# Performance work log

Measured on AMD Instinct MI355X. Metric: run time of the kernel, lower is better.

## Reference

```python
import jax, jax.numpy as jnp
import numpy as np

DN = ('NCDHW', 'OIDHW', 'NCDHW')

def conv3d(x, w, b, stride=1, padding=1, lhs_dilation=1):
    pad = [(padding, padding)] * 3 if isinstance(padding, int) else padding
    y = jax.lax.conv_general_dilated(
        x, w, window_strides=(stride,) * 3, padding=pad,
        lhs_dilation=(lhs_dilation,) * 3, dimension_numbers=DN)
    return y + b[None, :, None, None, None]

def bool_to_multichannel(x):
    # (B,1,D,H,W) bool -> (B,8,D/4,H/4,W/4) float; each 4x4x4 patch bit-packed to 8 bytes
    B = x.shape[0]; D = x.shape[2]; d = D // 4
    p = x.reshape(B, d, 4, d, 4, d, 4)
    p = p.transpose(0, 1, 3, 5, 2, 4, 6).reshape(B, d, d, d, 8, 8)
    pw2 = (2.0 ** jnp.arange(8)).astype(jnp.float32)
    mc = jnp.sum(p.astype(jnp.float32) * pw2, axis=-1)  # (B,d,d,d,8)
    return mc.transpose(0, 4, 1, 2, 3) / 255.0

def setup_inputs():
    key = jax.random.key(0)
    ks = jax.random.split(key, 26)
    B, RES = 4, 256
    CH, E, ZC, K = 32, 16, 128, 8192
    L = 16  # latent resolution (mc res 64 / 2^(len(ch_mult)-1))
    # block-sparse boolean voxels so a good fraction of latent patches is all-zero
    coarse = jax.random.uniform(ks[0], (B, 1, 16, 16, 16)) < 0.6
    coarse = jnp.repeat(jnp.repeat(jnp.repeat(coarse, 16, 2), 16, 3), 16, 4)
    dense = jax.random.uniform(ks[1], (B, 1, RES, RES, RES)) < 0.3
    x = coarse & dense
    p = lambda k, shape, s=0.05: (jax.random.normal(k, shape) * s).astype(jnp.float32)
    return {
        'x': x,
        'enc_in_w': p(ks[2], (CH, 8, 3, 3, 3)), 'enc_in_b': p(ks[3], (CH,)),
        'enc_d1_w': p(ks[4], (2 * CH, CH, 3, 3, 3)), 'enc_d1_b': p(ks[5], (2 * CH,)),
        'enc_d2_w': p(ks[6], (4 * CH, 2 * CH, 3, 3, 3)), 'enc_d2_b': p(ks[7], (4 * CH,)),
        'enc_out_w': p(ks[8], (ZC, 4 * CH, 3, 3, 3)), 'enc_out_b': p(ks[9], (ZC,)),
        'quant_w': p(ks[10], (E, ZC, 1, 1, 1)), 'quant_b': p(ks[11], (E,)),
        'codebook': p(ks[12], (K, E), 0.5),
        'replacement_token': p(ks[13], (1, E), 0.02),
        'pos_embedding': p(ks[14], (1, E, L, L, L), 1.0),
        'post_quant_w': p(ks[15], (ZC, E, 1, 1, 1)), 'post_quant_b': p(ks[16], (ZC,)),
        'dec_in_w': p(ks[17], (ZC, ZC, 3, 3, 3)), 'dec_in_b': p(ks[18], (ZC,)),
        'dec_u1_w': p(ks[19], (2 * CH, ZC, 3, 3, 3)), 'dec_u1_b': p(ks[20], (2 * CH,)),
        'dec_u2_w': p(ks[21], (CH, 2 * CH, 3, 3, 3)), 'dec_u2_b': p(ks[22], (CH,)),
        'dec_out_w': p(ks[23], (8, CH, 3, 3, 3)), 'dec_out_b': p(ks[24], (8,)),
    }

def reference(x, enc_in_w, enc_in_b, enc_d1_w, enc_d1_b, enc_d2_w, enc_d2_b,
              enc_out_w, enc_out_b, quant_w, quant_b, codebook, replacement_token,
              pos_embedding, post_quant_w, post_quant_b, dec_in_w, dec_in_b,
              dec_u1_w, dec_u1_b, dec_u2_w, dec_u2_b, dec_out_w, dec_out_b):
    silu = jax.nn.silu
    mc = bool_to_multichannel(x)                      # (B,8,64,64,64)
    B, _, Dm, _, _ = mc.shape
    L = Dm // 4                                       # latent res = 16

    # zero-patch mask, patch_size=4 (== max_pool3d(nonzero_any) < 0.5)
    nz = jnp.any(mc != 0, axis=1)                     # (B,64,64,64)
    pooled = nz.reshape(B, L, 4, L, 4, L, 4).any(axis=(2, 4, 6))
    zero_mask = ~pooled.reshape(B, L * L * L)         # (B,N) True = all-zero patch

    # encoder (downsample x4) + quant_conv (1x1x1)
    h = silu(conv3d(mc, enc_in_w, enc_in_b))
    h = silu(conv3d(h, enc_d1_w, enc_d1_b, stride=2))
    h = silu(conv3d(h, enc_d2_w, enc_d2_b, stride=2))
    h = conv3d(h, enc_out_w, enc_out_b)
    h = conv3d(h, quant_w, quant_b, padding=0)        # (B,E,L,L,L)
    E = h.shape[1]
    seq = h.reshape(B, E, -1).transpose(0, 2, 1)      # (B,N,E)

    dist = jnp.sum(codebook * codebook, axis=-1) - 2.0 * jnp.einsum('bne,ke->bnk', seq, codebook)
    idx = jnp.argmin(dist, axis=-1)                   # (B,N)
    q_nz = codebook[idx]                              # (B,N,E)
    nonzero = ~zero_mask
    # commit over nonzero tokens * non_mask_frac == masked mean over all tokens
    mse_tok = jnp.mean(jnp.square(jax.lax.stop_gradient(q_nz) - seq), axis=-1)
    commit_loss = 0.25 * jnp.mean(jnp.where(nonzero, mse_tok, 0.0))

    # replacement token is index 0 of the full codebook; real codes shift by +1
    full_idx = jnp.where(zero_mask, 0, idx + 1)       # (B,N)
    full_cb = jnp.concatenate([replacement_token, codebook], axis=0)
    quant = full_cb[full_idx].transpose(0, 2, 1).reshape(B, E, L, L, L)

    # decoder (upsample x4 via fractionally-strided convs)
    q = quant + pos_embedding
    q = conv3d(q, post_quant_w, post_quant_b, padding=0)
    d = silu(conv3d(q, dec_in_w, dec_in_b))
    d = silu(conv3d(d, dec_u1_w, dec_u1_b, padding=[(2, 1)] * 3, lhs_dilation=2))
    d = silu(conv3d(d, dec_u2_w, dec_u2_b, padding=[(2, 1)] * 3, lhs_dilation=2))
    recon = conv3d(d, dec_out_w, dec_out_b)           # (B,8,64,64,64)
    return recon, mc, commit_loss, full_idx
```

## Files before the change

kernel.cpp:

```cpp
#include <hip/hip_runtime.h>
#include <hip/hip_bf16.h>
#include <math.h>

#define BB 4
#define NTOK 4096
#define KCB 8192
#define ED 16

__device__ __forceinline__ float silu_f(float x){ return x / (1.0f + expf(-x)); }
__device__ __forceinline__ double silu_d(double x){ return x / (1.0 + exp(-x)); }

template<typename T> struct V4T { typedef T type __attribute__((ext_vector_type(4))); };
typedef float f2v __attribute__((ext_vector_type(2)));

__global__ void r9_probe_zero(int* flags){ if (threadIdx.x < 2) flags[threadIdx.x] = 0; }

__global__ void r17_probe(const unsigned char* __restrict__ x, int* __restrict__ flags){
  __shared__ int so, sa;
  if (threadIdx.x == 0){ so = 0; sa = 0; }
  __syncthreads();
  const uint4* p = (const uint4*)x + (size_t)(blockIdx.x*256 + threadIdx.x)*4;
  unsigned uo = 0, ua = 0;
  #pragma unroll
  for (int r=0;r<4;++r){
    uint4 v = p[r];
    unsigned uw = v.x | v.y | v.z | v.w;
    uo |= (uw & 0xFFFFFF00u);
    ua |= (uw & 0x000000FFu);
  }
  if (uo) so = 1;
  if (ua) sa = 1;
  __syncthreads();
  if (threadIdx.x == 0){
    if (so) atomicOr(flags + 0, 1);
    if (sa) atomicOr(flags + 1, 1);
  }
}

__global__ void r9_pack_mc(const unsigned char* __restrict__ x, float* __restrict__ mc,
                           const int* __restrict__ flags){
  int t = blockIdx.x*256 + threadIdx.x;
  int k = t & 63, j = (t>>6)&63, i = (t>>12)&63, b = t>>18;
  int is_i32 = (flags[1] != 0) && (flags[0] == 0);
  unsigned ch[8];
  #pragma unroll
  for (int q=0;q<8;++q) ch[q]=0u;
  if (is_i32){
    const int* xb = (const int*)x + ((size_t)b << 24);
    #pragma unroll
    for (int a=0;a<4;++a){
      #pragma unroll
      for (int b2=0;b2<4;++b2){
        const int4 v = *(const int4*)(xb + (((size_t)(4*i+a))<<16) + ((size_t)(4*j+b2)<<8) + (size_t)(4*k));
        int vv[4] = {v.x, v.y, v.z, v.w};
        #pragma unroll
        for (int c2=0;c2<4;++c2){
          int lin = a*16 + b2*4 + c2;
          unsigned bit = vv[c2] ? 1u : 0u;
          ch[lin>>3] += bit << (lin&7);
        }
      }
    }
  } else {
    const unsigned char* xb = x + ((size_t)b << 24);
    #pragma unroll
    for (int a=0;a<4;++a){
      #pragma unroll
      for (int b2=0;b2<4;++b2){
        const unsigned char* row = xb + (((size_t)(4*i+a))<<16) + ((size_t)(4*j+b2)<<8) + (size_t)(4*k);
        unsigned v = *(const unsigned*)row;
        #pragma unroll
        for (int c2=0;c2<4;++c2){
          int lin = a*16 + b2*4 + c2;
          unsigned bit = ((v >> (8*c2)) & 0xffu) ? 1u : 0u;
          ch[lin>>3] += bit << (lin&7);
        }
      }
    }
  }
  size_t sp = ((size_t)i<<12) + (j<<6) + k;
  #pragma unroll
  for (int q=0;q<8;++q)
    mc[(((size_t)(b*8+q))<<18) + sp] = (float)ch[q] / 255.0f;
}

__global__ void r9_token_nz(const float* __restrict__ mc, unsigned char* __restrict__ tnz){
  int t = blockIdx.x*64 + threadIdx.x;
  int tk = t&15, tj=(t>>4)&15, ti=(t>>8)&15, b=t>>12;
  bool any = false;
  for (int q=0;q<8 && !any;++q){
    const float* mq = mc + (((size_t)(b*8+q))<<18);
    for (int a=0;a<4;++a)
      for (int c=0;c<4;++c){
        const float4 v = *(const float4*)(mq + ((size_t)(4*ti+a)<<12) + ((size_t)(4*tj+c)<<6) + (size_t)(4*tk));
        if (v.x!=0.f || v.y!=0.f || v.z!=0.f || v.w!=0.f){ any = true; }
      }
  }
  tnz[t] = any ? 1 : 0;
}

template<int XT, int STRIDE, typename TIN, typename ACC>
__device__ __forceinline__ void load_span(const TIN* __restrict__ inr, bool xlo, bool xhi,
                                          ACC (&xv)[STRIDE*(XT-1)+3]){
  static_assert(XT==4, "XT must be 4");
  typedef typename V4T<TIN>::type tin4;
  if (STRIDE==1){
    tin4 m = *(const tin4*)(inr + 1);
    xv[1]=(ACC)m.x; xv[2]=(ACC)m.y; xv[3]=(ACC)m.z; xv[4]=(ACC)m.w;
    xv[0] = xlo ? (ACC)inr[0] : (ACC)0;
    xv[5] = xhi ? (ACC)inr[5] : (ACC)0;
  } else {
    tin4 a = *(const tin4*)(inr + 1);
    tin4 b = *(const tin4*)(inr + 5);
    xv[1]=(ACC)a.x; xv[2]=(ACC)a.y; xv[3]=(ACC)a.z; xv[4]=(ACC)a.w;
    xv[5]=(ACC)b.x; xv[6]=(ACC)b.y; xv[7]=(ACC)b.z; xv[8]=(ACC)b.w;
    xv[0] = xlo ? (ACC)inr[0] : (ACC)0;
  }
}

template<int CIN, int OCB, int XT, int STRIDE, bool DOSILU, typename TIN, typename TOUT, typename ACC>
__global__ void r16_conv3x3(const TIN* __restrict__ in, const float* __restrict__ w,
                            const float* __restrict__ bias, TOUT* __restrict__ out,
                            int Din, int Dout){
  constexpr int SPAN = STRIDE*(XT-1)+3;
  const int oc0 = blockIdx.y * OCB;
  const int n3 = Dout*Dout*Dout;
  const int nxt = Dout / XT;
  const int t = blockIdx.x*256 + threadIdx.x;
  const int xo0 = (t % nxt)*XT;
  const int yo = (t/nxt)%Dout, zo = t/(nxt*Dout);
  const int zi0 = zo*STRIDE-1, yi0 = yo*STRIDE-1, xi0 = xo0*STRIDE-1;
  const bool xlo = (xi0 >= 0);
  const bool xhi = (xi0 + (SPAN-1) < Din);

  ACC acc[OCB][XT];
  #pragma unroll
  for (int q=0;q<OCB;++q){
    ACC bv = (ACC)bias[oc0+q];
    #pragma unroll
    for (int s=0;s<XT;++s) acc[q][s] = bv;
  }

  #pragma unroll 1
  for (int i=0;i<CIN;++i){
    const TIN* inc = in + (size_t)i*Din*Din*Din;
    const float* wci = w + ((size_t)oc0*CIN + i)*27;
    #pragma unroll
    for (int kd=0;kd<3;++kd){
      int z = zi0+kd; if ((unsigned)z >= (unsigned)Din) continue;
      #pragma unroll
      for (int kh=0;kh<3;++kh){
        int y = yi0+kh; if ((unsigned)y >= (unsigned)Din) continue;
        const TIN* inr = inc + ((size_t)z*Din + y)*Din + xi0;
        ACC xv[SPAN];
        load_span<XT,STRIDE,TIN,ACC>(inr, xlo, xhi, xv);
        #pragma unroll
        for (int q=0;q<OCB;++q){
          const float* wr = wci + (size_t)q*CIN*27 + kd*9 + kh*3;
          #pragma unroll
          for (int kw=0;kw<3;++kw){
            ACC wv = (ACC)wr[kw];
            #pragma unroll
            for (int s=0;s<XT;++s)
              acc[q][s] = fma(wv, xv[s*STRIDE+kw], acc[q][s]);
          }
        }
      }
    }
  }
  if (DOSILU){
    #pragma unroll
    for (int q=0;q<OCB;++q)
      #pragma unroll
      for (int s=0;s<XT;++s){
        if (sizeof(ACC)==8) acc[q][s] = (ACC)silu_d((double)acc[q][s]);
        else                acc[q][s] = (ACC)silu_f((float)acc[q][s]);
      }
  }
  size_t vox = ((size_t)zo*Dout + yo)*Dout + xo0;
  #pragma unroll
  for (int q=0;q<OCB;++q)
    #pragma unroll
    for (int s=0;s<XT;++s)
      out[(size_t)(oc0+q)*n3 + vox + s] = (TOUT)acc[q][s];
}

template<int CIN, int OCB, int XT, int NS, int STRIDE, typename TIN, typename ACC>
__global__ void r16_conv_part(const TIN* __restrict__ in, const float* __restrict__ w,
                              const float* __restrict__ bias, ACC* __restrict__ part,
                              int Din, int Dout){
  constexpr int SPAN = STRIDE*(XT-1)+3;
  const int oc0 = blockIdx.y * OCB;
  const int OC  = gridDim.y * OCB;
  const int cz  = blockIdx.z;
  const int n3 = Dout*Dout*Dout;
  const int nxt = Dout / XT;
  const int t = blockIdx.x*256 + threadIdx.x;
  const int xo0 = (t % nxt)*XT;
  const int yo = (t/nxt)%Dout, zo = t/(nxt*Dout);
  const int zi0 = zo*STRIDE-1, yi0 = yo*STRIDE-1, xi0 = xo0*STRIDE-1;
  const bool xlo = (xi0 >= 0);
  const bool xhi = (xi0 + (SPAN-1) < Din);

  ACC acc[OCB][XT];
  #pragma unroll
  for (int q=0;q<OCB;++q){
    ACC bv = (cz==0) ? (ACC)bias[oc0+q] : (ACC)0;
    #pragma unroll
    for (int s=0;s<XT;++s) acc[q][s] = bv;
  }

  const int cbeg = cz * (CIN/NS);
  #pragma unroll 1
  for (int i=cbeg; i<cbeg + CIN/NS; ++i){
    const TIN* inc = in + (size_t)i*Din*Din*Din;
    const float* wci = w + ((size_t)oc0*CIN + i)*27;
    #pragma unroll
    for (int kd=0;kd<3;++kd){
      int z = zi0+kd; if ((unsigned)z >= (unsigned)Din) continue;
      #pragma unroll
      for (int kh=0;kh<3;++kh){
        int y = yi0+kh; if ((unsigned)y >= (unsigned)Din) continue;
        const TIN* inr = inc + ((size_t)z*Din + y)*Din + xi0;
        ACC xv[SPAN];
        load_span<XT,STRIDE,TIN,ACC>(inr, xlo, xhi, xv);
        #pragma unroll
        for (int q=0;q<OCB;++q){
          const float* wr = wci + (size_t)q*CIN*27 + kd*9 + kh*3;
          #pragma unroll
          for (int kw=0;kw<3;++kw){
            ACC wv = (ACC)wr[kw];
            #pragma unroll
            for (int s=0;s<XT;++s)
              acc[q][s] = fma(wv, xv[s*STRIDE+kw], acc[q][s]);
          }
        }
      }
    }
  }
  size_t vox = ((size_t)zo*Dout + yo)*Dout + xo0;
  #pragma unroll
  for (int q=0;q<OCB;++q)
    #pragma unroll
    for (int s=0;s<XT;++s)
      part[((size_t)cz*OC + (oc0+q))*n3 + vox + s] = acc[q][s];
}

template<int NS, int VEC, bool DOSILU, typename ACC, typename TOUT>
__global__ void r16_reduce(const ACC* __restrict__ part, TOUT* __restrict__ out, int total){
  int t0 = (blockIdx.x*256 + threadIdx.x)*VEC;
  if (t0 >= total) return;
  ACC a[VEC];
  #pragma unroll
  for (int v=0;v<VEC;++v) a[v] = part[t0+v];
  #pragma unroll
  for (int s=1;s<NS;++s){
    #pragma unroll
    for (int v=0;v<VEC;++v) a[v] += part[(size_t)s*total + t0+v];
  }
  #pragma unroll
  for (int v=0;v<VEC;++v){
    if (DOSILU){
      if (sizeof(ACC)==8) a[v] = (ACC)silu_d((double)a[v]);
      else                a[v] = (ACC)silu_f((float)a[v]);
    }
    out[t0+v] = (TOUT)a[v];
  }
}

__global__ void r9_quantconv_b(const double* __restrict__ h4b, const float* __restrict__ w,
                               const float* __restrict__ bias, double* __restrict__ seqd, int b){
  int t = blockIdx.x*256 + threadIdx.x;
  if (t >= 65536) return;
  int n = t & 4095, e = t >> 12;
  double acc = (double)bias[e];
  const float* we = w + e*128;
  for (int i=0;i<128;++i) acc = fma(h4b[((size_t)i<<12)+n], (double)we[i], acc);
  seqd[((size_t)(b*NTOK+n))*ED + e] = acc;
}

__global__ void r9_postquant_b(const float* __restrict__ qpeb, const float* __restrict__ w,
                               const float* __restrict__ bias, float* __restrict__ pqb){
  int t = blockIdx.x*256 + threadIdx.x;
  if (t >= 524288) return;
  int n = t & 4095, o = t >> 12;
  float acc = bias[o];
  const float* wo = w + o*16;
  #pragma unroll
  for (int e=0;e<16;++e) acc = fmaf(qpeb[((size_t)e<<12)+n], wo[e], acc);
  pqb[t] = acc;
}

__global__ void r9_cnorm(const float* __restrict__ cb, double* __restrict__ cnormd){
  int k = blockIdx.x*256 + threadIdx.x;
  if (k >= KCB) return;
  const float* c = cb + (size_t)k*ED;
  double s = 0.0;
  #pragma unroll
  for (int e=0;e<ED;++e) s = fma((double)c[e], (double)c[e], s);
  cnormd[k] = s;
}

#define VQC 256
#define VQPARTS 16
template<int PARTS>
__global__ void r12_vq_partial(const double* __restrict__ seqd, const float* __restrict__ cb,
                               const double* __restrict__ cnormd,
                               double* __restrict__ pdist, int* __restrict__ pidx){
  __shared__ double scb[VQC*ED];
  __shared__ double snorm[VQC];
  int part = blockIdx.y;
  int tok = blockIdx.x*256 + threadIdx.x;
  double s[16];
  const double* sr = seqd + (size_t)tok*ED;
  #pragma unroll
  for (int e=0;e<16;++e) s[e] = sr[e];
  double best = 1.0e300; int bi = 0;
  const int CP = KCB/PARTS;
  for (int c=0;c<CP/VQC;++c){
    int kbase = part*CP + c*VQC;
    for (int u=threadIdx.x; u<VQC*ED; u+=256) scb[u] = (double)cb[(size_t)kbase*ED + u];
    for (int u=threadIdx.x; u<VQC; u+=256) snorm[u] = cnormd[kbase+u];
    __syncthreads();
    for (int kk=0; kk<VQC; ++kk){
      const double* cr = scb + kk*ED;
      double dot = 0.0;
      #pragma unroll
      for (int e=0;e<16;++e) dot = fma(s[e], cr[e], dot);
      double dist = snorm[kk] - 2.0*dot;
      if (dist < best){ best = dist; bi = kbase+kk; }
    }
    __syncthreads();
  }
  pdist[part*16384 + tok] = best;
  pidx [part*16384 + tok] = bi;
}

template<int PARTS>
__global__ void r12_vq_merge(const double* __restrict__ pdist, const int* __restrict__ pidx,
                             const unsigned char* __restrict__ tnz, int* __restrict__ idxw,
                             float* __restrict__ out_idx, float* __restrict__ loss_slot){
  int tok = blockIdx.x*256 + threadIdx.x;
  if (tok == 0) *loss_slot = 0.f;
  double best = pdist[tok]; int bi = pidx[tok];
  #pragma unroll
  for (int p=1;p<PARTS;++p){
    double d2 = pdist[p*16384+tok];
    if (d2 < best){ best = d2; bi = pidx[p*16384+tok]; }
  }
  idxw[tok] = bi;
  out_idx[tok] = tnz[tok] ? (float)(bi+1) : 0.f;
}

__global__ void r9_commit(const double* __restrict__ seqd, const float* __restrict__ cb,
                          const int* __restrict__ idxw, const unsigned char* __restrict__ tnz,
                          float* __restrict__ loss_slot){
  int tok = blockIdx.x*256 + threadIdx.x;
  float v = 0.f;
  if (tnz[tok]){
    const float* c = cb + (size_t)idxw[tok]*ED;
    const double* s = seqd + (size_t)tok*ED;
    double acc = 0.0;
    #pragma unroll
    for (int e=0;e<ED;++e){ double d = (double)c[e]-s[e]; acc = fma(d,d,acc); }
    v = (float)(acc * (0.25/(16.0*16384.0)));
  }
  #pragma unroll
  for (int off=32; off; off>>=1) v += __shfl_down(v, off);
  if ((threadIdx.x & 63) == 0) atomicAdd(loss_slot, v);
}

__global__ void r9_gather_pos(const float* __restrict__ cb, const float* __restrict__ rep,
                              const int* __restrict__ idxw, const unsigned char* __restrict__ tnz,
                              const float* __restrict__ pos, float* __restrict__ qpe){
  int t = blockIdx.x*256 + threadIdx.x;
  int n = t & 4095, e = (t>>12)&15, b = t>>16;
  int tok = b*NTOK + n;
  float v = tnz[tok] ? cb[(size_t)idxw[tok]*ED + e] : rep[e];
  qpe[t] = v + pos[((size_t)e<<12) + n];
}

template<int CIN, int XT, bool DOSILU>
__global__ void r16_tconv(const float* __restrict__ in, const float* __restrict__ w,
                          const float* __restrict__ bias, float* __restrict__ out,
                          int Din){
  static_assert(XT==2, "XT must be 2");
  const int oc = blockIdx.y;
  const int nxt = Din / XT;
  const int t = blockIdx.x*256 + threadIdx.x;
  const int ux0 = (t % nxt)*XT;
  const int uy = (t/nxt)%Din, uz = t/(nxt*Din);
  const bool vx = ux0 > 0, vy = uy > 0, vz = uz > 0;
  const int DD = Din*Din, n3 = DD*Din;

  float b0 = bias[oc];
  float acc[8][XT];
  #pragma unroll
  for (int q=0;q<8;++q)
    #pragma unroll
    for (int s=0;s<XT;++s) acc[q][s] = b0;

  const float* p = in + ((size_t)uz*Din + uy)*Din + ux0;
  #pragma unroll 1
  for (int i=0;i<CIN;++i){
    float X[2][2][XT+1];
    #pragma unroll
    for (int za=0; za<2; ++za){
      #pragma unroll
      for (int ya=0; ya<2; ++ya){
        bool okzy = (za==1 || vz) && (ya==1 || vy);
        const float* pr = p + (za-1)*DD + (ya-1)*Din;
        if (okzy){
          f2v m = *(const f2v*)(pr);
          X[za][ya][1] = m.x; X[za][ya][2] = m.y;
          X[za][ya][0] = vx ? pr[-1] : 0.f;
        } else {
          X[za][ya][0] = 0.f; X[za][ya][1] = 0.f; X[za][ya][2] = 0.f;
        }
      }
    }
    const float* wi = w + ((size_t)(oc*CIN) + i)*27;
    #pragma unroll
    for (int kd=0;kd<3;++kd){
      #pragma unroll
      for (int kh=0;kh<3;++kh){
        #pragma unroll
        for (int kw=0;kw<3;++kw){
          const int pz = (kd==1) ? 1 : 0, py = (kh==1) ? 1 : 0, px = (kw==1) ? 1 : 0;
          const int za = (kd==0) ? 0 : 1, ya = (kh==0) ? 0 : 1, xa = (kw==0) ? 0 : 1;
          float wv = wi[kd*9+kh*3+kw];
          #pragma unroll
          for (int s=0;s<XT;++s)
            acc[pz*4+py*2+px][s] = fmaf(wv, X[za][ya][s+xa], acc[pz*4+py*2+px][s]);
        }
      }
    }
    p += n3;
  }
  if (DOSILU){
    #pragma unroll
    for (int q=0;q<8;++q)
      #pragma unroll
      for (int s=0;s<XT;++s) acc[q][s] = silu_f(acc[q][s]);
  }
  const int Dout = 2*Din;
  #pragma unroll
  for (int pz=0; pz<2; ++pz){
    #pragma unroll
    for (int py=0; py<2; ++py){
      float* row = out + (((size_t)oc*Dout + 2*uz+pz)*Dout + (2*uy+py))*Dout + 2*ux0;
      #pragma unroll
      for (int s=0;s<XT;++s){
        float2 v2 = make_float2(acc[pz*4+py*2+0][s], acc[pz*4+py*2+1][s]);
        *(float2*)(row + 2*s) = v2;
      }
    }
  }
}

template<int CIN, int XT, int NS>
__global__ void r16_tconv_part(const float* __restrict__ in, const float* __restrict__ w,
                               const float* __restrict__ bias, float* __restrict__ part,
                               int Din){
  static_assert(XT==2, "XT must be 2");
  const int oc = blockIdx.y;
  const int OC = gridDim.y;
  const int cz = blockIdx.z;
  const int nxt = Din / XT;
  const int t = blockIdx.x*256 + threadIdx.x;
  const int ux0 = (t % nxt)*XT;
  const int uy = (t/nxt)%Din, uz = t/(nxt*Din);
  const bool vx = ux0 > 0, vy = uy > 0, vz = uz > 0;
  const int DD = Din*Din, n3 = DD*Din;

  float b0 = (cz==0) ? bias[oc] : 0.f;
  float acc[8][XT];
  #pragma unroll
  for (int q=0;q<8;++q)
    #pragma unroll
    for (int s=0;s<XT;++s) acc[q][s] = b0;

  const int cbeg = cz * (CIN/NS);
  const float* p = in + (size_t)cbeg*n3 + ((size_t)uz*Din + uy)*Din + ux0;
  #pragma unroll 1
  for (int i=cbeg; i<cbeg + CIN/NS; ++i){
    float X[2][2][XT+1];
    #pragma unroll
    for (int za=0; za<2; ++za){
      #pragma unroll
      for (int ya=0; ya<2; ++ya){
        bool okzy = (za==1 || vz) && (ya==1 || vy);
        const float* pr = p + (za-1)*DD + (ya-1)*Din;
        if (okzy){
          f2v m = *(const f2v*)(pr);
          X[za][ya][1] = m.x; X[za][ya][2] = m.y;
          X[za][ya][0] = vx ? pr[-1] : 0.f;
        } else {
          X[za][ya][0] = 0.f; X[za][ya][1] = 0.f; X[za][ya][2] = 0.f;
        }
      }
    }
    const float* wi = w + ((size_t)(oc*CIN) + i)*27;
    #pragma unroll
    for (int kd=0;kd<3;++kd){
      #pragma unroll
      for (int kh=0;kh<3;++kh){
        #pragma unroll
        for (int kw=0;kw<3;++kw){
          const int pz = (kd==1) ? 1 : 0, py = (kh==1) ? 1 : 0, px = (kw==1) ? 1 : 0;
          const int za = (kd==0) ? 0 : 1, ya = (kh==0) ? 0 : 1, xa = (kw==0) ? 0 : 1;
          float wv = wi[kd*9+kh*3+kw];
          #pragma unroll
          for (int s=0;s<XT;++s)
            acc[pz*4+py*2+px][s] = fmaf(wv, X[za][ya][s+xa], acc[pz*4+py*2+px][s]);
        }
      }
    }
    p += n3;
  }
  const int Dout = 2*Din;
  const size_t n3out = (size_t)Dout*Dout*Dout;
  float* pb = part + (size_t)cz*OC*n3out;
  #pragma unroll
  for (int pz=0; pz<2; ++pz){
    #pragma unroll
    for (int py=0; py<2; ++py){
      float* row = pb + (((size_t)oc*Dout + 2*uz+pz)*Dout + (2*uy+py))*Dout + 2*ux0;
      #pragma unroll
      for (int s=0;s<XT;++s){
        float2 v2 = make_float2(acc[pz*4+py*2+0][s], acc[pz*4+py*2+1][s]);
        *(float2*)(row + 2*s) = v2;
      }
    }
  }
}

__global__ void r9_diag_ws(float* out0, float v){
  if (threadIdx.x == 0 && blockIdx.x == 0) out0[0] = v;
}

extern "C" void kernel_launch(void* const* d_in, const int* in_sizes, int n_in,
                              void* d_out, int out_size, void* d_ws, size_t ws_size,
                              hipStream_t stream){
  const unsigned char* x = (const unsigned char*)d_in[0];
  const float* enc_in_w  = (const float*)d_in[1];
  const float* enc_in_b  = (const float*)d_in[2];
  const float* enc_d1_w  = (const float*)d_in[3];
  const float* enc_d1_b  = (const float*)d_in[4];
  const float* enc_d2_w  = (const float*)d_in[5];
  const float* enc_d2_b  = (const float*)d_in[6];
  const float* enc_out_w = (const float*)d_in[7];
  const float* enc_out_b = (const float*)d_in[8];
  const float* quant_w   = (const float*)d_in[9];
  const float* quant_b   = (const float*)d_in[10];
  const float* codebook  = (const float*)d_in[11];
  const float* rep_tok   = (const float*)d_in[12];
  const float* pos_emb   = (const float*)d_in[13];
  const float* pq_w      = (const float*)d_in[14];
  const float* pq_b      = (const float*)d_in[15];
  const float* dec_in_w  = (const float*)d_in[16];
  const float* dec_in_b  = (const float*)d_in[17];
  const float* dec_u1_w  = (const float*)d_in[18];
  const float* dec_u1_b  = (const float*)d_in[19];
  const float* dec_u2_w  = (const float*)d_in[20];
  const float* dec_u2_b  = (const float*)d_in[21];
  const float* dec_out_w = (const float*)d_in[22];
  const float* dec_out_b = (const float*)d_in[23];

  float* out = (float*)d_out;
  const size_t OFF_RECON = 0;
  const size_t OFF_MC    = 8388608;
  const size_t OFF_LOSS  = 16777216;
  const size_t OFF_IDX   = 16777217;

  char* wsb = (char*)d_ws;
  float*  Sbig  = (float*) (wsb + 0);
  float*  Shd   = (float*) (wsb + 33554432);
  double* Sc1   = (double*)(wsb + 41943040);
  double* Sc2   = (double*)(wsb + 46137344);
  float*  Spq   = (float*) (wsb + 50331648);
  float*  SdD   = (float*) (wsb + 52428800);
  double* seqd  = (double*)(wsb + 54525952);
  double* cnormd= (double*)(wsb + 56623104);
  int*    idxw  = (int*)   (wsb + 57475072);
  unsigned char* tnz = (unsigned char*)(wsb + 57540608);
  float*  qpe   = (float*) (wsb + 57556992);
  int*    dflag = (int*)   (wsb + 58605568);
  const size_t WS_NEEDED = 58605632;

  double* scr_d  = (double*)wsb;
  float*  scr_f  = (float*)wsb;
  float*  scr_f2 = (float*)(wsb + 33554432);
  double* pdist  = (double*)wsb;
  int*    pidx   = (int*)(wsb + VQPARTS*16384*8);

  dim3 blk(256);

  if (ws_size < WS_NEEDED){
    r9_diag_ws<<<dim3(1), dim3(64), 0, stream>>>(out + OFF_RECON,
        9.0e6f + (float)(ws_size >> 20));
    return;
  }

  r9_probe_zero<<<dim3(1), dim3(64), 0, stream>>>(dflag);
  r17_probe<<<dim3(256), blk, 0, stream>>>(x, dflag);

  r9_pack_mc<<<dim3(4096), blk, 0, stream>>>(x, out + OFF_MC, dflag);
  r9_token_nz<<<dim3(256), dim3(64), 0, stream>>>(out + OFF_MC, tnz);

  for (int b = 0; b < BB; ++b){
    const float* mcb = out + OFF_MC + (size_t)b*8*262144;
    r16_conv3x3<8,8,4,1,true,float,float,double>  <<<dim3(256,4,1), blk, 0, stream>>>(mcb,  enc_in_w, enc_in_b, Sbig, 64, 64);
    r16_conv3x3<32,4,4,2,true,float,float,double> <<<dim3(32,16,1), blk, 0, stream>>>(Sbig, enc_d1_w, enc_d1_b, Shd,  64, 32);
    r16_conv_part<64,4,4,4,2,float,double><<<dim3(4,32,4), blk, 0, stream>>>(Shd, enc_d2_w, enc_d2_b, scr_d, 32, 16);
    r16_reduce<4,2,true,double,double><<<dim3(1024), blk, 0, stream>>>(scr_d, Sc1, 524288);
    r16_conv_part<128,4,4,8,1,double,double><<<dim3(4,32,8), blk, 0, stream>>>(Sc1, enc_out_w, enc_out_b, scr_d, 16, 16);
    r16_reduce<8,2,false,double,double><<<dim3(1024), blk, 0, stream>>>(scr_d, Sc2, 524288);
    r9_quantconv_b<<<dim3(256), blk, 0, stream>>>(Sc2, quant_w, quant_b, seqd, b);
  }

  r9_cnorm<<<dim3(32), blk, 0, stream>>>(codebook, cnormd);
  r12_vq_partial<VQPARTS><<<dim3(64,VQPARTS), blk, 0, stream>>>(seqd, codebook, cnormd, pdist, pidx);
  r12_vq_merge<VQPARTS><<<dim3(64), blk, 0, stream>>>(pdist, pidx, tnz, idxw, out + OFF_IDX, out + OFF_LOSS);
  r9_commit<<<dim3(64), blk, 0, stream>>>(seqd, codebook, idxw, tnz, out + OFF_LOSS);

  r9_gather_pos<<<dim3(1024), blk, 0, stream>>>(codebook, rep_tok, idxw, tnz, pos_emb, qpe);
  for (int b = 0; b < BB; ++b){
    const float* qpeb = qpe + (size_t)b*65536;
    float* reconb = out + OFF_RECON + (size_t)b*8*262144;
    r9_postquant_b<<<dim3(2048), blk, 0, stream>>>(qpeb, pq_w, pq_b, Spq);
    r16_conv_part<128,4,4,8,1,float,float><<<dim3(4,32,8), blk, 0, stream>>>(Spq, dec_in_w, dec_in_b, scr_f, 16, 16);
    r16_reduce<8,4,true,float,float><<<dim3(512), blk, 0, stream>>>(scr_f, SdD, 524288);
    r16_tconv_part<128,2,2><<<dim3(8,64,2), blk, 0, stream>>>(SdD, dec_u1_w, dec_u1_b, scr_f2, 16);
    r16_reduce<2,4,true,float,float><<<dim3(2048), blk, 0, stream>>>(scr_f2, Shd, 2097152);
    r16_tconv<64,2,true> <<<dim3(64,32,1), blk, 0, stream>>>(Shd,  dec_u2_w, dec_u2_b, Sbig, 32);
    r16_conv_part<32,8,4,2,1,float,float><<<dim3(256,1,2), blk, 0, stream>>>(Sbig, dec_out_w, dec_out_b, scr_f2, 64, 64);
    r16_reduce<2,4,false,float,float><<<dim3(2048), blk, 0, stream>>>(scr_f2, reconb, 2097152);
  }
}
```

Measured before the change: 3.836 ms.

## Batch encoder down-convs across batch, fold final reduce into quantconv, retile VQ

```diff
diff --git a/kernel.cpp b/kernel.cpp
--- a/kernel.cpp
+++ b/kernel.cpp
@@ -246,6 +246,69 @@
       part[((size_t)cz*OC + (oc0+q))*n3 + vox + s] = acc[q][s];
 }
 
+template<int CIN, int OCB, int XT, int NS, int STRIDE, typename TIN, typename ACC>
+__global__ void r18_conv_part_b(const TIN* __restrict__ in_all, size_t in_bstride,
+                                const float* __restrict__ w, const float* __restrict__ bias,
+                                ACC* __restrict__ part, int Din, int Dout){
+  constexpr int SPAN = STRIDE*(XT-1)+3;
+  const int oc0 = blockIdx.y * OCB;
+  const int OC  = gridDim.y * OCB;
+  const int bz  = blockIdx.z / NS;
+  const int cz  = blockIdx.z % NS;
+  const TIN* in = in_all + (size_t)bz*in_bstride;
+  const int n3 = Dout*Dout*Dout;
+  const int nxt = Dout / XT;
+  const int t = blockIdx.x*256 + threadIdx.x;
+  const int xo0 = (t % nxt)*XT;
+  const int yo = (t/nxt)%Dout, zo = t/(nxt*Dout);
+  const int zi0 = zo*STRIDE-1, yi0 = yo*STRIDE-1, xi0 = xo0*STRIDE-1;
+  const bool xlo = (xi0 >= 0);
+  const bool xhi = (xi0 + (SPAN-1) < Din);
+
+  ACC acc[OCB][XT];
+  #pragma unroll
+  for (int q=0;q<OCB;++q){
+    ACC bv = (cz==0) ? (ACC)bias[oc0+q] : (ACC)0;
+    #pragma unroll
+    for (int s=0;s<XT;++s) acc[q][s] = bv;
+  }
+
+  const int cbeg = cz * (CIN/NS);
+  #pragma unroll 1
+  for (int i=cbeg; i<cbeg + CIN/NS; ++i){
+    const TIN* inc = in + (size_t)i*Din*Din*Din;
+    const float* wci = w + ((size_t)oc0*CIN + i)*27;
+    #pragma unroll
+    for (int kd=0;kd<3;++kd){
+      int z = zi0+kd; if ((unsigned)z >= (unsigned)Din) continue;
+      #pragma unroll
+      for (int kh=0;kh<3;++kh){
+        int y = yi0+kh; if ((unsigned)y >= (unsigned)Din) continue;
+        const TIN* inr = inc + ((size_t)z*Din + y)*Din + xi0;
+        ACC xv[SPAN];
+        load_span<XT,STRIDE,TIN,ACC>(inr, xlo, xhi, xv);
+        #pragma unroll
+        for (int q=0;q<OCB;++q){
+          const float* wr = wci + (size_t)q*CIN*27 + kd*9 + kh*3;
+          #pragma unroll
+          for (int kw=0;kw<3;++kw){
+            ACC wv = (ACC)wr[kw];
+            #pragma unroll
+            for (int s=0;s<XT;++s)
+              acc[q][s] = fma(wv, xv[s*STRIDE+kw], acc[q][s]);
+          }
+        }
+      }
+    }
+  }
+  size_t vox = ((size_t)zo*Dout + yo)*Dout + xo0;
+  #pragma unroll
+  for (int q=0;q<OCB;++q)
+    #pragma unroll
+    for (int s=0;s<XT;++s)
+      part[((size_t)(bz*NS+cz)*OC + (oc0+q))*n3 + vox + s] = acc[q][s];
+}
+
 template<int NS, int VEC, bool DOSILU, typename ACC, typename TOUT>
 __global__ void r16_reduce(const ACC* __restrict__ part, TOUT* __restrict__ out, int total){
   int t0 = (blockIdx.x*256 + threadIdx.x)*VEC;
@@ -268,14 +331,40 @@
   }
 }
 
-__global__ void r9_quantconv_b(const double* __restrict__ h4b, const float* __restrict__ w,
-                               const float* __restrict__ bias, double* __restrict__ seqd, int b){
+template<int NS, int VEC, bool DOSILU, typename ACC, typename TOUT>
+__global__ void r18_reduce_b(const ACC* __restrict__ part, TOUT* __restrict__ out, int total){
+  int b = blockIdx.y;
+  int t0 = (blockIdx.x*256 + threadIdx.x)*VEC;
+  if (t0 >= total) return;
+  const ACC* pb = part + (size_t)b*NS*total;
+  ACC a[VEC];
+  #pragma unroll
+  for (int v=0;v<VEC;++v) a[v] = pb[t0+v];
+  #pragma unroll
+  for (int s=1;s<NS;++s){
+    #pragma unroll
+    for (int v=0;v<VEC;++v) a[v] += pb[(size_t)s*total + t0+v];
+  }
+  #pragma unroll
+  for (int v=0;v<VEC;++v){
+    if (DOSILU){
+      if (sizeof(ACC)==8) a[v] = (ACC)silu_d((double)a[v]);
+      else                a[v] = (ACC)silu_f((float)a[v]);
+    }
+    out[(size_t)b*total + t0+v] = (TOUT)a[v];
+  }
+}
+
+__global__ void r18_quantconv(const double* __restrict__ parts, const float* __restrict__ w,
+                              const float* __restrict__ bias, double* __restrict__ seqd){
   int t = blockIdx.x*256 + threadIdx.x;
-  if (t >= 65536) return;
-  int n = t & 4095, e = t >> 12;
+  int n = t & 4095, e = (t>>12)&15, b = t>>16;
+  const double* p0 = parts + (size_t)(b*2+0)*524288 + n;
+  const double* p1 = parts + (size_t)(b*2+1)*524288 + n;
   double acc = (double)bias[e];
   const float* we = w + e*128;
-  for (int i=0;i<128;++i) acc = fma(h4b[((size_t)i<<12)+n], (double)we[i], acc);
+  for (int i=0;i<128;++i)
+    acc = fma(p0[(size_t)i<<12] + p1[(size_t)i<<12], (double)we[i], acc);
   seqd[((size_t)(b*NTOK+n))*ED + e] = acc;
 }
 
@@ -302,38 +391,45 @@
 }
 
 #define VQC 256
-#define VQPARTS 16
+#define VQPARTS 32
 template<int PARTS>
-__global__ void r12_vq_partial(const double* __restrict__ seqd, const float* __restrict__ cb,
+__global__ void r18_vq_partial(const double* __restrict__ seqd, const float* __restrict__ cb,
                                const double* __restrict__ cnormd,
                                double* __restrict__ pdist, int* __restrict__ pidx){
   __shared__ double scb[VQC*ED];
   __shared__ double snorm[VQC];
-  int part = blockIdx.y;
-  int tok = blockIdx.x*256 + threadIdx.x;
-  double s[16];
-  const double* sr = seqd + (size_t)tok*ED;
-  #pragma unroll
-  for (int e=0;e<16;++e) s[e] = sr[e];
-  double best = 1.0e300; int bi = 0;
-  const int CP = KCB/PARTS;
-  for (int c=0;c<CP/VQC;++c){
-    int kbase = part*CP + c*VQC;
-    for (int u=threadIdx.x; u<VQC*ED; u+=256) scb[u] = (double)cb[(size_t)kbase*ED + u];
-    for (int u=threadIdx.x; u<VQC; u+=256) snorm[u] = cnormd[kbase+u];
-    __syncthreads();
-    for (int kk=0; kk<VQC; ++kk){
-      const double* cr = scb + kk*ED;
-      double dot = 0.0;
-      #pragma unroll
-      for (int e=0;e<16;++e) dot = fma(s[e], cr[e], dot);
-      double dist = snorm[kk] - 2.0*dot;
-      if (dist < best){ best = dist; bi = kbase+kk; }
-    }
-    __syncthreads();
-  }
-  pdist[part*16384 + tok] = best;
-  pidx [part*16384 + tok] = bi;
+  const int part = blockIdx.y;
+  const int tok0 = blockIdx.x*256 + threadIdx.x;
+  const int tok1 = tok0 + 8192;
+  double s0[16], s1[16];
+  const double* sr0 = seqd + (size_t)tok0*ED;
+  const double* sr1 = seqd + (size_t)tok1*ED;
+  #pragma unroll
+  for (int e=0;e<16;++e){ s0[e] = sr0[e]; s1[e] = sr1[e]; }
+  const int kbase = part * (KCB/PARTS);
+  for (int u=threadIdx.x; u<VQC*ED; u+=256) scb[u] = (double)cb[(size_t)kbase*ED + u];
+  for (int u=threadIdx.x; u<VQC; u+=256) snorm[u] = cnormd[kbase+u];
+  __syncthreads();
+  double best0 = 1.0e300, best1 = 1.0e300; int bi0 = 0, bi1 = 0;
+  for (int kk=0; kk<VQC; ++kk){
+    const double* cr = scb + kk*ED;
+    double dot0 = 0.0, dot1 = 0.0;
+    #pragma unroll
+    for (int e=0;e<16;++e){
+      double c = cr[e];
+      dot0 = fma(s0[e], c, dot0);
+      dot1 = fma(s1[e], c, dot1);
+    }
+    double nm = snorm[kk];
+    double d0 = nm - 2.0*dot0;
+    double d1 = nm - 2.0*dot1;
+    if (d0 < best0){ best0 = d0; bi0 = kbase+kk; }
+    if (d1 < best1){ best1 = d1; bi1 = kbase+kk; }
+  }
+  pdist[part*16384 + tok0] = best0;
+  pidx [part*16384 + tok0] = bi0;
+  pdist[part*16384 + tok1] = best1;
+  pidx [part*16384 + tok1] = bi1;
 }
 
 template<int PARTS>
@@ -576,8 +672,6 @@
   char* wsb = (char*)d_ws;
   float*  Sbig  = (float*) (wsb + 0);
   float*  Shd   = (float*) (wsb + 33554432);
-  double* Sc1   = (double*)(wsb + 41943040);
-  double* Sc2   = (double*)(wsb + 46137344);
   float*  Spq   = (float*) (wsb + 50331648);
   float*  SdD   = (float*) (wsb + 52428800);
   double* seqd  = (double*)(wsb + 54525952);
@@ -591,8 +685,10 @@
   double* scr_d  = (double*)wsb;
   float*  scr_f  = (float*)wsb;
   float*  scr_f2 = (float*)(wsb + 33554432);
+  double* h3     = (double*)(wsb + 33554432);
   double* pdist  = (double*)wsb;
   int*    pidx   = (int*)(wsb + VQPARTS*16384*8);
+  float* h2all = out + OFF_RECON;
 
   dim3 blk(256);
 
@@ -611,16 +707,15 @@
   for (int b = 0; b < BB; ++b){
     const float* mcb = out + OFF_MC + (size_t)b*8*262144;
     r16_conv3x3<8,8,4,1,true,float,float,double>  <<<dim3(256,4,1), blk, 0, stream>>>(mcb,  enc_in_w, enc_in_b, Sbig, 64, 64);
-    r16_conv3x3<32,4,4,2,true,float,float,double> <<<dim3(32,16,1), blk, 0, stream>>>(Sbig, enc_d1_w, enc_d1_b, Shd,  64, 32);
-    r16_conv_part<64,4,4,4,2,float,double><<<dim3(4,32,4), blk, 0, stream>>>(Shd, enc_d2_w, enc_d2_b, scr_d, 32, 16);
-    r16_reduce<4,2,true,double,double><<<dim3(1024), blk, 0, stream>>>(scr_d, Sc1, 524288);
-    r16_conv_part<128,4,4,8,1,double,double><<<dim3(4,32,8), blk, 0, stream>>>(Sc1, enc_out_w, enc_out_b, scr_d, 16, 16);
-    r16_reduce<8,2,false,double,double><<<dim3(1024), blk, 0, stream>>>(scr_d, Sc2, 524288);
-    r9_quantconv_b<<<dim3(256), blk, 0, stream>>>(Sc2, quant_w, quant_b, seqd, b);
-  }
+    r16_conv3x3<32,4,4,2,true,float,float,double> <<<dim3(32,16,1), blk, 0, stream>>>(Sbig, enc_d1_w, enc_d1_b, h2all + (size_t)b*2097152, 64, 32);
+  }
+  r18_conv_part_b<64,4,4,2,2,float,double><<<dim3(4,32,8), blk, 0, stream>>>(h2all, 2097152, enc_d2_w, enc_d2_b, scr_d, 32, 16);
+  r18_reduce_b<2,2,true,double,double><<<dim3(1024,4), blk, 0, stream>>>(scr_d, h3, 524288);
+  r18_conv_part_b<128,4,4,2,1,double,double><<<dim3(4,32,8), blk, 0, stream>>>(h3, 524288, enc_out_w, enc_out_b, scr_d, 16, 16);
+  r18_quantconv<<<dim3(1024), blk, 0, stream>>>(scr_d, quant_w, quant_b, seqd);
 
   r9_cnorm<<<dim3(32), blk, 0, stream>>>(codebook, cnormd);
-  r12_vq_partial<VQPARTS><<<dim3(64,VQPARTS), blk, 0, stream>>>(seqd, codebook, cnormd, pdist, pidx);
+  r18_vq_partial<VQPARTS><<<dim3(32,VQPARTS), blk, 0, stream>>>(seqd, codebook, cnormd, pdist, pidx);
   r12_vq_merge<VQPARTS><<<dim3(64), blk, 0, stream>>>(pdist, pidx, tnz, idxw, out + OFF_IDX, out + OFF_LOSS);
   r9_commit<<<dim3(64), blk, 0, stream>>>(seqd, codebook, idxw, tnz, out + OFF_LOSS);
 
```

New measurement: 3.676 ms. 4.2% less time.
